# Performance work log

Hardware: AMD Instinct MI355X
Metric: run time of the kernel (lower is better)

The kernel has to match this reference:

```python
import jax, jax.numpy as jnp
import numpy as np

N = 80000       # nodes
E = 1280000     # edges (avg degree 16)
G = 2000        # graphs
NSHAPE, NCOLOR, POSMAX = 16, 16, 1024
HID, OUT, IN_DIM = 64, 2, 40
EPS = 1e-5


def setup_inputs() -> dict:
    key = jax.random.key(0)
    ks = jax.random.split(key, 20)
    f32 = jnp.float32
    return {
        "shape_id": jax.random.randint(ks[0], (N,), 0, NSHAPE),
        "color_id": jax.random.randint(ks[1], (N,), 0, NCOLOR),
        "pos_id": jax.random.randint(ks[2], (N,), 0, POSMAX),
        "edge_index": jax.random.randint(ks[3], (2, E), 0, N),
        "batch": jnp.sort(jax.random.randint(ks[4], (N,), 0, G)),
        "num_graphs": G,
        "shape_tab": jax.random.normal(ks[5], (NSHAPE, 16), f32),
        "color_tab": jax.random.normal(ks[6], (NCOLOR, 16), f32),
        "pos_tab": jax.random.normal(ks[7], (POSMAX, 8), f32),
        "W1l": jax.random.normal(ks[8], (IN_DIM, HID), f32) / np.sqrt(IN_DIM),
        "b1": jnp.zeros((HID,), f32),
        "W1r": jax.random.normal(ks[9], (IN_DIM, HID), f32) / np.sqrt(IN_DIM),
        "g1": jnp.ones((HID,), f32),
        "be1": jnp.zeros((HID,), f32),
        "W2l": jax.random.normal(ks[10], (HID, HID), f32) / np.sqrt(HID),
        "b2": jnp.zeros((HID,), f32),
        "W2r": jax.random.normal(ks[11], (HID, HID), f32) / np.sqrt(HID),
        "g2": jnp.ones((HID,), f32),
        "be2": jnp.zeros((HID,), f32),
        "Wout": jax.random.normal(ks[12], (HID, OUT), f32) / np.sqrt(HID),
        "bout": jnp.zeros((OUT,), f32),
    }


def sage_conv(x, src, dst, Wl, b, Wr, n_nodes):
    # PyG SAGEConv (mean aggr): out = lin_l(mean_{j in N(i)} x_j) + lin_r(x_i)
    agg = jax.ops.segment_sum(x[src], dst, num_segments=n_nodes)     # [N, F]
    deg = jax.ops.segment_sum(jnp.ones((src.shape[0], 1), x.dtype), dst,
                              num_segments=n_nodes)                  # [N, 1]
    agg = agg / jnp.maximum(deg, 1.0)
    return agg @ Wl + b + x @ Wr


def batch_norm(x, gamma, beta):
    # training-mode BatchNorm1d over nodes
    m = x.mean(axis=0)
    v = x.var(axis=0)
    return (x - m) * (gamma / jnp.sqrt(v + EPS)) + beta


def reference(shape_id, color_id, pos_id, edge_index, batch, num_graphs,
              shape_tab, color_tab, pos_tab,
              W1l, b1, W1r, g1, be1,
              W2l, b2, W2r, g2, be2,
              Wout, bout):
    n_nodes = shape_id.shape[0]
    src, dst = edge_index[0], edge_index[1]
    x = jnp.concatenate([shape_tab[shape_id], color_tab[color_id],
                         pos_tab[pos_id]], axis=-1)                  # [N, 40]
    x = jax.nn.relu(batch_norm(sage_conv(x, src, dst, W1l, b1, W1r, n_nodes), g1, be1))
    # dropout: eval mode -> identity
    x = jax.nn.relu(batch_norm(sage_conv(x, src, dst, W2l, b2, W2r, n_nodes), g2, be2))
    # global mean pool over batch segments
    summed = jax.ops.segment_sum(x, batch, num_segments=num_graphs)   # [G, H]
    counts = jax.ops.segment_sum(jnp.ones((n_nodes, 1), x.dtype), batch,
                                 num_segments=num_graphs)
    pooled = summed / jnp.maximum(counts, 1.0)
    return pooled @ Wout + bout                                       # [G, 2]
```

## Files before the change

### kernel.cpp

```cpp
#include <hip/hip_runtime.h>

#define NN 80000
#define NE 1280000
#define NG 2000
#define HID 64
#define FIN1 40
#define BSZ 128
#define NBUK (NN / BSZ)
#define EB 8192
#define NBB ((NE + EB - 1) / EB)
#define NBBP 160
constexpr float EPS = 1e-5f;

typedef _Float16 f16;
typedef f16 f16x8 __attribute__((ext_vector_type(8)));
typedef float f32x4 __attribute__((ext_vector_type(4)));

__global__ void setup(const int* __restrict__ sid, const int* __restrict__ cid,
                      const int* __restrict__ pid, const int* __restrict__ batch,
                      const float* __restrict__ stab, const float* __restrict__ ctab,
                      const float* __restrict__ ptab,
                      const float* __restrict__ W1l, const float* __restrict__ W1r,
                      const float* __restrict__ W2l, const float* __restrict__ W2r,
                      int* __restrict__ ids, f16* __restrict__ Bt1, f16* __restrict__ Bt2,
                      int* __restrict__ gstart,
                      f16* __restrict__ stab16, f16* __restrict__ ctab16,
                      f16* __restrict__ ptab16) {
    int bid = blockIdx.x;
    int tid = threadIdx.x;
    if (bid < 313) {
        int n = bid * 256 + tid;
        if (n < NN) ids[n] = sid[n] | (cid[n] << 4) | (pid[n] << 8);
    } else if (bid < 373) {
        int i = (bid - 313) * 256 + tid;
        if (i < 64 * 104) {
            int j = i / 104, k = i - j * 104;
            float v = 0.f;
            if (k < 40) v = W1l[k * 64 + j];
            else if (k < 80) v = W1r[(k - 40) * 64 + j];
            Bt1[i] = (f16)v;
        }
        int i2 = i - 64 * 104;
        if (i2 >= 0 && i2 < 64 * 136) {
            int j = i2 / 136, k = i2 - j * 136;
            float v = 0.f;
            if (k < 64) v = W2l[k * 64 + j];
            else if (k < 128) v = W2r[(k - 64) * 64 + j];
            Bt2[i2] = (f16)v;
        }
    } else if (bid < 686) {
        int n = (bid - 373) * 256 + tid;
        if (n >= NN) return;
        int cur = batch[n];
        int prev = (n == 0) ? -1 : batch[n - 1];
        for (int g = prev + 1; g <= cur; g++) gstart[g] = n;
        if (n == NN - 1)
            for (int g = cur + 1; g <= NG; g++) gstart[g] = NN;
    } else {
        int i = (bid - 686) * 256 + tid;
        if (i < 256) stab16[i] = (f16)stab[i];
        else if (i < 512) ctab16[i - 256] = (f16)ctab[i - 256];
        else if (i < 512 + 8192) ptab16[i - 512] = (f16)ptab[i - 512];
    }
}

__global__ void khist(const int* __restrict__ dst, int* __restrict__ bhistT,
                      int* __restrict__ bcnt) {
    __shared__ int lh[NBUK];
    for (int i = threadIdx.x; i < NBUK; i += 256) lh[i] = 0;
    __syncthreads();
    int e0 = blockIdx.x * EB, e1 = min(e0 + EB, NE);
    for (int e = e0 + threadIdx.x; e < e1; e += 256) atomicAdd(&lh[dst[e] >> 7], 1);
    __syncthreads();
    for (int i = threadIdx.x; i < NBUK; i += 256) {
        int c = lh[i];
        bhistT[i * NBBP + blockIdx.x] = c;
        if (c) atomicAdd(&bcnt[i], c);
    }
}

__global__ void kscan_a(const int* __restrict__ bcnt, int* __restrict__ bstart) {
    __shared__ int l[1024];
    int t = threadIdx.x;
    l[t] = (t < NBUK) ? bcnt[t] : 0;
    __syncthreads();
    for (int off = 1; off < 1024; off <<= 1) {
        int v = (t >= off) ? l[t - off] : 0;
        __syncthreads();
        l[t] += v;
        __syncthreads();
    }
    if (t < NBUK) bstart[t] = (t == 0) ? 0 : l[t - 1];
    if (t == NBUK) bstart[NBUK] = NE;
}

__global__ void kscan_b(const int* __restrict__ bhistT, const int* __restrict__ bstart,
                        int* __restrict__ lbaseT) {
    int b = blockIdx.x;
    int l = threadIdx.x;
    int run = bstart[b];
    for (int i0 = 0; i0 < NBB; i0 += 64) {
        int idx = i0 + l;
        int v = (idx < NBB) ? bhistT[b * NBBP + idx] : 0;
        int inc = v;
        for (int off = 1; off < 64; off <<= 1) {
            int tt = __shfl_up(inc, off);
            if (l >= off) inc += tt;
        }
        if (idx < NBB) lbaseT[b * NBBP + idx] = run + inc - v;
        run += __shfl(inc, 63);
    }
}

__global__ void kbin(const int* __restrict__ src, const int* __restrict__ dst,
                     const int* __restrict__ lbaseT, int* __restrict__ ebuf) {
    __shared__ int lcur[NBUK];
    for (int i = threadIdx.x; i < NBUK; i += 256) lcur[i] = lbaseT[i * NBBP + blockIdx.x];
    __syncthreads();
    int e0 = blockIdx.x * EB, e1 = min(e0 + EB, NE);
    for (int e = e0 + threadIdx.x; e < e1; e += 256) {
        int d = dst[e];
        int off = atomicAdd(&lcur[d >> 7], 1);
        ebuf[off] = (src[e] << 7) | (d & 127);
    }
}

__global__ void kfill(const int* __restrict__ ebuf, const int* __restrict__ bstart,
                      int* __restrict__ row_ptr, int* __restrict__ eidx) {
    __shared__ int cnt[BSZ];
    __shared__ int sb[BSZ];
    __shared__ int lcur[BSZ];
    int b = blockIdx.x, t = threadIdx.x;
    int nbase = b << 7;
    if (t < BSZ) cnt[t] = 0;
    __syncthreads();
    int s0 = bstart[b], s1 = bstart[b + 1];
    for (int i = s0 + t; i < s1; i += 256) atomicAdd(&cnt[ebuf[i] & 127], 1);
    __syncthreads();
    if (t < BSZ) sb[t] = cnt[t];
    __syncthreads();
    for (int off = 1; off < BSZ; off <<= 1) {
        int v = (t >= off && t < BSZ) ? sb[t - off] : 0;
        __syncthreads();
        if (t < BSZ) sb[t] += v;
        __syncthreads();
    }
    if (t < BSZ) {
        int excl = ((t == 0) ? 0 : sb[t - 1]) + s0;
        row_ptr[nbase + t] = excl;
        lcur[t] = excl;
    }
    if (b == 0 && t == 0) row_ptr[NN] = NE;
    __syncthreads();
    for (int i = s0 + t; i < s1; i += 256) {
        int v = ebuf[i];
        int pos = atomicAdd(&lcur[v & 127], 1);
        eidx[pos] = v >> 7;
    }
}

__global__ void gather1(const int* __restrict__ row_ptr, const int* __restrict__ eidx,
                        const int* __restrict__ ids,
                        const f16* __restrict__ stab16, const f16* __restrict__ ctab16,
                        const f16* __restrict__ ptab16, f16* __restrict__ agg) {
    int tt = blockIdx.x * 256 + threadIdx.x;
    int n = tt >> 6;
    int lane = threadIdx.x & 63;
    if (n >= NN) return;
    int grp = lane >> 3, li = lane & 7;
    int beg = row_ptr[n], end = row_ptr[n + 1];
    float ac[8];
#pragma unroll
    for (int i = 0; i < 8; i++) ac[i] = 0.f;
    for (int j0 = beg; j0 < end; j0 += 64) {
        int cnt = min(64, end - j0);
        int myid = (j0 + lane < end) ? eidx[j0 + lane] : 0;
        int steps = (cnt + 7) >> 3;
        for (int u = 0; u < steps; u++) {
            int e = u * 8 + grp;
            int s = __shfl(myid, e);
            if (e < cnt && li < 5) {
                int id = ids[s];
                const f16* rowp;
                if (li < 2)      rowp = &stab16[(id & 15) * 16 + li * 8];
                else if (li < 4) rowp = &ctab16[((id >> 4) & 15) * 16 + (li - 2) * 8];
                else             rowp = &ptab16[(id >> 8) * 8];
                f16x8 v = *(const f16x8*)rowp;
#pragma unroll
                for (int i = 0; i < 8; i++) ac[i] += (float)v[i];
            }
        }
    }
#pragma unroll
    for (int m = 8; m <= 32; m <<= 1) {
#pragma unroll
        for (int i = 0; i < 8; i++) ac[i] += __shfl_xor(ac[i], m);
    }
    if (lane < 5) {
        f16x8 o;
#pragma unroll
        for (int i = 0; i < 8; i++) o[i] = (f16)ac[i];
        *(f16x8*)&agg[(size_t)n * FIN1 + lane * 8] = o;
    }
}

__global__ void gather2(const int* __restrict__ row_ptr, const int* __restrict__ eidx,
                        const f16* __restrict__ x, const float* __restrict__ stats,
                        const float* __restrict__ g1, const float* __restrict__ be1,
                        f16* __restrict__ agg) {
    int tt = blockIdx.x * 256 + threadIdx.x;
    int n = tt >> 6;
    int lane = threadIdx.x & 63;
    if (n >= NN) return;
    int grp = lane >> 3;
    int fl = (lane & 7) * 8;
    float sc8[8], sh8[8];
    {
        const float invn = 1.0f / (float)NN;
#pragma unroll
        for (int i = 0; i < 8; i++) {
            float m = stats[fl + i] * invn;
            float var = stats[64 + fl + i] * invn - m * m;
            float sc = g1[fl + i] * __frsqrt_rn(var + EPS);
            sc8[i] = sc;
            sh8[i] = be1[fl + i] - m * sc;
        }
    }
    int beg = row_ptr[n], end = row_ptr[n + 1];
    float ac[8];
#pragma unroll
    for (int i = 0; i < 8; i++) ac[i] = 0.f;
    for (int j0 = beg; j0 < end; j0 += 64) {
        int cnt = min(64, end - j0);
        int myid = (j0 + lane < end) ? eidx[j0 + lane] : 0;
        int steps = (cnt + 7) >> 3;
        for (int u = 0; u < steps; u++) {
            int e = u * 8 + grp;
            int s = __shfl(myid, e);
            if (e < cnt) {
                f16x8 v = *(const f16x8*)&x[(size_t)s * HID + fl];
#pragma unroll
                for (int i = 0; i < 8; i++)
                    ac[i] += fmaxf(fmaf((float)v[i], sc8[i], sh8[i]), 0.f);
            }
        }
    }
#pragma unroll
    for (int m = 8; m <= 32; m <<= 1) {
#pragma unroll
        for (int i = 0; i < 8; i++) ac[i] += __shfl_xor(ac[i], m);
    }
    if (lane < 8) {
        f16x8 o;
#pragma unroll
        for (int i = 0; i < 8; i++) o[i] = (f16)ac[i];
        *(f16x8*)&agg[(size_t)n * HID + fl] = o;
    }
}

__launch_bounds__(256)
__global__ void sage_mfma1(const int* __restrict__ ids, const f16* __restrict__ agg,
                           const int* __restrict__ row_ptr,
                           const f16* __restrict__ stab16, const f16* __restrict__ ctab16,
                           const f16* __restrict__ ptab16,
                           const f16* __restrict__ Btg, const float* __restrict__ bias,
                           f16* __restrict__ h, float* __restrict__ stats) {
    const int KTOT = 96, KP = 104, UT = KP / 8;
    __shared__ f16 Asm[64 * KP];
    __shared__ f16 Bsm[64 * KP];
    __shared__ float sinv[64];
    __shared__ float sred[4][64];
    __shared__ float qred[4][64];

    int tid = threadIdx.x;
    int n0 = blockIdx.x * 64;
    if (tid < 64) {
        int n = n0 + tid;
        int deg = row_ptr[n + 1] - row_ptr[n];
        sinv[tid] = 1.0f / (float)max(deg, 1);
    }
    __syncthreads();

    for (int i = tid; i < 64 * UT; i += 256) {
        int r = i / UT, u = i - r * UT;
        f16x8 o;
        if (u < 5) {
            f16x8 va = *(const f16x8*)&agg[(size_t)(n0 + r) * FIN1 + u * 8];
            float inv = sinv[r];
#pragma unroll
            for (int k = 0; k < 8; k++) o[k] = (f16)((float)va[k] * inv);
        } else if (u < 10) {
            int id = ids[n0 + r];
            int c = u - 5;
            const f16* rowp;
            if (c < 2)      rowp = &stab16[(id & 15) * 16 + c * 8];
            else if (c < 4) rowp = &ctab16[((id >> 4) & 15) * 16 + (c - 2) * 8];
            else            rowp = &ptab16[(id >> 8) * 8];
            o = *(const f16x8*)rowp;
        } else {
#pragma unroll
            for (int k = 0; k < 8; k++) o[k] = (f16)0.f;
        }
        *(f16x8*)&Asm[r * KP + u * 8] = o;
    }
    for (int i = tid; i < 64 * KP * 2 / 16; i += 256)
        ((uint4*)Bsm)[i] = ((const uint4*)Btg)[i];
    __syncthreads();

    int w = tid >> 6, l = tid & 63;
    int jloc = l & 15, kg = l >> 4;
    int rbase = w * 16;
    f32x4 acc[4];
#pragma unroll
    for (int jt = 0; jt < 4; jt++) {
        float bj = bias[jt * 16 + jloc];
        acc[jt] = (f32x4){bj, bj, bj, bj};
    }
#pragma unroll
    for (int kk = 0; kk < KTOT / 32; kk++) {
        f16x8 af = *(const f16x8*)&Asm[(rbase + jloc) * KP + kk * 32 + kg * 8];
#pragma unroll
        for (int jt = 0; jt < 4; jt++) {
            f16x8 bf = *(const f16x8*)&Bsm[(jt * 16 + jloc) * KP + kk * 32 + kg * 8];
            acc[jt] = __builtin_amdgcn_mfma_f32_16x16x32_f16(af, bf, acc[jt], 0, 0, 0);
        }
    }
#pragma unroll
    for (int jt = 0; jt < 4; jt++) {
        float sv = 0.f, qv = 0.f;
#pragma unroll
        for (int reg = 0; reg < 4; reg++) {
            f16 hv = (f16)acc[jt][reg];
            int n = n0 + rbase + kg * 4 + reg;
            h[(size_t)n * HID + jt * 16 + jloc] = hv;
            float v = (float)hv;
            sv += v; qv += v * v;
        }
        sv += __shfl_xor(sv, 16); sv += __shfl_xor(sv, 32);
        qv += __shfl_xor(qv, 16); qv += __shfl_xor(qv, 32);
        if (kg == 0) { sred[w][jt * 16 + jloc] = sv; qred[w][jt * 16 + jloc] = qv; }
    }
    __syncthreads();
    if (tid < 128) {
        int f2 = tid & 63, which = tid >> 6;
        float r = which ? (qred[0][f2] + qred[1][f2] + qred[2][f2] + qred[3][f2])
                        : (sred[0][f2] + sred[1][f2] + sred[2][f2] + sred[3][f2]);
        atomicAdd(&stats[which * 64 + f2], r);
    }
}

__launch_bounds__(256)
__global__ void sage_mfma2(const f16* __restrict__ x, const f16* __restrict__ agg,
                           const int* __restrict__ row_ptr, const f16* __restrict__ Btg,
                           const float* __restrict__ bias, f16* __restrict__ h,
                           const float* __restrict__ stats1, const float* __restrict__ g1,
                           const float* __restrict__ be1, float* __restrict__ stats) {
    const int FIN = 64, KTOT = 128, KP = 136, UT = KP / 8;
    __shared__ f16 Asm[64 * KP];
    __shared__ f16 Bsm[64 * KP];
    __shared__ float sinv[64];
    __shared__ float ssc[64], ssh[64];
    __shared__ float sred[4][64];
    __shared__ float qred[4][64];

    int tid = threadIdx.x;
    int n0 = blockIdx.x * 64;
    if (tid < 64) {
        int n = n0 + tid;
        int deg = row_ptr[n + 1] - row_ptr[n];
        sinv[tid] = 1.0f / (float)max(deg, 1);
        const float invn = 1.0f / (float)NN;
        float m = stats1[tid] * invn;
        float var = stats1[64 + tid] * invn - m * m;
        float sc = g1[tid] * __frsqrt_rn(var + EPS);
        ssc[tid] = sc;
        ssh[tid] = be1[tid] - m * sc;
    }
    __syncthreads();

    for (int i = tid; i < 64 * UT; i += 256) {
        int r = i / UT, u = i - r * UT;
        f16x8 o;
        if (u < 8) {
            f16x8 va = *(const f16x8*)&agg[(size_t)(n0 + r) * FIN + u * 8];
            float inv = sinv[r];
#pragma unroll
            for (int k = 0; k < 8; k++) o[k] = (f16)((float)va[k] * inv);
        } else if (u < 16) {
            int fb = (u - 8) * 8;
            f16x8 vx = *(const f16x8*)&x[(size_t)(n0 + r) * FIN + fb];
#pragma unroll
            for (int k = 0; k < 8; k++)
                o[k] = (f16)fmaxf(fmaf((float)vx[k], ssc[fb + k], ssh[fb + k]), 0.f);
        } else {
#pragma unroll
            for (int k = 0; k < 8; k++) o[k] = (f16)0.f;
        }
        *(f16x8*)&Asm[r * KP + u * 8] = o;
    }
    for (int i = tid; i < 64 * KP * 2 / 16; i += 256)
        ((uint4*)Bsm)[i] = ((const uint4*)Btg)[i];
    __syncthreads();

    int w = tid >> 6, l = tid & 63;
    int jloc = l & 15, kg = l >> 4;
    int rbase = w * 16;
    f32x4 acc[4];
#pragma unroll
    for (int jt = 0; jt < 4; jt++) {
        float bj = bias[jt * 16 + jloc];
        acc[jt] = (f32x4){bj, bj, bj, bj};
    }
#pragma unroll
    for (int kk = 0; kk < KTOT / 32; kk++) {
        f16x8 af = *(const f16x8*)&Asm[(rbase + jloc) * KP + kk * 32 + kg * 8];
#pragma unroll
        for (int jt = 0; jt < 4; jt++) {
            f16x8 bf = *(const f16x8*)&Bsm[(jt * 16 + jloc) * KP + kk * 32 + kg * 8];
            acc[jt] = __builtin_amdgcn_mfma_f32_16x16x32_f16(af, bf, acc[jt], 0, 0, 0);
        }
    }
#pragma unroll
    for (int jt = 0; jt < 4; jt++) {
        float sv = 0.f, qv = 0.f;
#pragma unroll
        for (int reg = 0; reg < 4; reg++) {
            f16 hv = (f16)acc[jt][reg];
            int n = n0 + rbase + kg * 4 + reg;
            h[(size_t)n * HID + jt * 16 + jloc] = hv;
            float v = (float)hv;
            sv += v; qv += v * v;
        }
        sv += __shfl_xor(sv, 16); sv += __shfl_xor(sv, 32);
        qv += __shfl_xor(qv, 16); qv += __shfl_xor(qv, 32);
        if (kg == 0) { sred[w][jt * 16 + jloc] = sv; qred[w][jt * 16 + jloc] = qv; }
    }
    __syncthreads();
    if (tid < 128) {
        int f2 = tid & 63, which = tid >> 6;
        float r = which ? (qred[0][f2] + qred[1][f2] + qred[2][f2] + qred[3][f2])
                        : (sred[0][f2] + sred[1][f2] + sred[2][f2] + sred[3][f2]);
        atomicAdd(&stats[which * 64 + f2], r);
    }
}

__global__ void pool_out(const f16* __restrict__ h, const float* __restrict__ stats2,
                         const float* __restrict__ g2, const float* __restrict__ be2,
                         const int* __restrict__ gstart,
                         const float* __restrict__ Wout, const float* __restrict__ bout,
                         float* __restrict__ out) {
    int w = (blockIdx.x * blockDim.x + threadIdx.x) >> 6;
    int f = threadIdx.x & 63;
    if (w >= NG) return;
    const float invn = 1.0f / (float)NN;
    float m = stats2[f] * invn;
    float var = stats2[64 + f] * invn - m * m;
    float sc = g2[f] / sqrtf(var + EPS);
    float sh = be2[f] - m * sc;
    int n0 = gstart[w], n1 = gstart[w + 1];
    float acc = 0.f;
    for (int n = n0; n < n1; n++) {
        float v = fmaf((float)h[(size_t)n * HID + f], sc, sh);
        acc += fmaxf(v, 0.0f);
    }
    float inv = 1.0f / (float)max(n1 - n0, 1);
    float p = acc * inv;
    float a0 = p * Wout[f * 2 + 0];
    float a1 = p * Wout[f * 2 + 1];
#pragma unroll
    for (int mm = 1; mm < 64; mm <<= 1) {
        a0 += __shfl_xor(a0, mm);
        a1 += __shfl_xor(a1, mm);
    }
    if (f == 0) {
        out[w * 2 + 0] = a0 + bout[0];
        out[w * 2 + 1] = a1 + bout[1];
    }
}

extern "C" void kernel_launch(void* const* d_in, const int* in_sizes, int n_in,
                              void* d_out, int out_size, void* d_ws, size_t ws_size,
                              hipStream_t stream) {
    const int* sid = (const int*)d_in[0];
    const int* cid = (const int*)d_in[1];
    const int* pid = (const int*)d_in[2];
    const int* ei = (const int*)d_in[3];
    const int* batch = (const int*)d_in[4];
    const float* stab = (const float*)d_in[6];
    const float* ctab = (const float*)d_in[7];
    const float* ptab = (const float*)d_in[8];
    const float* W1l = (const float*)d_in[9];
    const float* b1 = (const float*)d_in[10];
    const float* W1r = (const float*)d_in[11];
    const float* g1 = (const float*)d_in[12];
    const float* be1 = (const float*)d_in[13];
    const float* W2l = (const float*)d_in[14];
    const float* b2 = (const float*)d_in[15];
    const float* W2r = (const float*)d_in[16];
    const float* g2 = (const float*)d_in[17];
    const float* be2 = (const float*)d_in[18];
    const float* Wout = (const float*)d_in[19];
    const float* bout = (const float*)d_in[20];

    const int* src = ei;
    const int* dst = ei + NE;

    char* p = (char*)d_ws;
    f16* agg = (f16*)p;        p += (size_t)NN * HID * 2;
    f16* h1 = (f16*)p;         p += (size_t)NN * HID * 2;
    f16* h2 = (f16*)p;         p += (size_t)NN * HID * 2;
    f16* bt1 = (f16*)p;        p += 64 * 104 * 2;
    f16* bt2 = (f16*)p;        p += 64 * 136 * 2;
    f16* stab16 = (f16*)p;     p += 256 * 2;
    f16* ctab16 = (f16*)p;     p += 256 * 2;
    f16* ptab16 = (f16*)p;     p += 8192 * 2;
    float* stats = (float*)p;  p += 256 * 4;
    int* bcnt = (int*)p;       p += NBUK * 4;
    int* ids = (int*)p;        p += (size_t)NN * 4;
    int* row_ptr = (int*)p;    p += (NN + 1) * 4;
    int* gstart = (int*)p;     p += (NG + 1) * 4;
    int* bstart = (int*)p;     p += (NBUK + 1) * 4;
    int* bhistT = (int*)p;     p += (size_t)NBUK * NBBP * 4;
    int* lbaseT = (int*)p;     p += (size_t)NBUK * NBBP * 4;
    int* ebuf = (int*)p;       p += (size_t)NE * 4;
    int* eidx = (int*)p;       p += (size_t)NE * 4;

    hipMemsetAsync(stats, 0, 256 * 4 + NBUK * 4, stream);

    const int B = 256;

    setup<<<720, B, 0, stream>>>(sid, cid, pid, batch, stab, ctab, ptab,
                                 W1l, W1r, W2l, W2r,
                                 ids, bt1, bt2, gstart, stab16, ctab16, ptab16);

    khist<<<NBB, B, 0, stream>>>(dst, bhistT, bcnt);
    kscan_a<<<1, 1024, 0, stream>>>(bcnt, bstart);
    kscan_b<<<NBUK, 64, 0, stream>>>(bhistT, bstart, lbaseT);
    kbin<<<NBB, B, 0, stream>>>(src, dst, lbaseT, ebuf);
    kfill<<<NBUK, B, 0, stream>>>(ebuf, bstart, row_ptr, eidx);

    gather1<<<(NN * 64 + B - 1) / B, B, 0, stream>>>(row_ptr, eidx, ids,
                                                     stab16, ctab16, ptab16, agg);
    sage_mfma1<<<NN / 64, B, 0, stream>>>(ids, agg, row_ptr, stab16, ctab16, ptab16,
                                          bt1, b1, h1, stats);

    gather2<<<(NN * 64 + B - 1) / B, B, 0, stream>>>(row_ptr, eidx, h1, stats, g1, be1, agg);
    sage_mfma2<<<NN / 64, B, 0, stream>>>(h1, agg, row_ptr, bt2, b2, h2,
                                          stats, g1, be1, stats + 128);

    pool_out<<<(NG * 64 + B - 1) / B, B, 0, stream>>>(h2, stats + 128, g2, be2, gstart,
                                                      Wout, bout, (float*)d_out);
}
```

Baseline: 237.9 us.

## Load MFMA operands directly from global memory and fold mean division into gathers

```diff
diff --git a/kernel.cpp b/kernel.cpp
--- a/kernel.cpp
+++ b/kernel.cpp
@@ -197,9 +197,10 @@
         for (int i = 0; i < 8; i++) ac[i] += __shfl_xor(ac[i], m);
     }
     if (lane < 5) {
+        float inv = 1.0f / (float)max(end - beg, 1);
         f16x8 o;
 #pragma unroll
-        for (int i = 0; i < 8; i++) o[i] = (f16)ac[i];
+        for (int i = 0; i < 8; i++) o[i] = (f16)(ac[i] * inv);
         *(f16x8*)&agg[(size_t)n * FIN1 + lane * 8] = o;
     }
 }
@@ -251,65 +252,50 @@
         for (int i = 0; i < 8; i++) ac[i] += __shfl_xor(ac[i], m);
     }
     if (lane < 8) {
+        float inv = 1.0f / (float)max(end - beg, 1);
         f16x8 o;
 #pragma unroll
-        for (int i = 0; i < 8; i++) o[i] = (f16)ac[i];
+        for (int i = 0; i < 8; i++) o[i] = (f16)(ac[i] * inv);
         *(f16x8*)&agg[(size_t)n * HID + fl] = o;
     }
 }
 
 __launch_bounds__(256)
-__global__ void sage_mfma1(const int* __restrict__ ids, const f16* __restrict__ agg,
-                           const int* __restrict__ row_ptr,
+__global__ void sage_mfma1(const int* __restrict__ ids, const f16* __restrict__ aggv,
                            const f16* __restrict__ stab16, const f16* __restrict__ ctab16,
                            const f16* __restrict__ ptab16,
                            const f16* __restrict__ Btg, const float* __restrict__ bias,
                            f16* __restrict__ h, float* __restrict__ stats) {
-    const int KTOT = 96, KP = 104, UT = KP / 8;
-    __shared__ f16 Asm[64 * KP];
-    __shared__ f16 Bsm[64 * KP];
-    __shared__ float sinv[64];
     __shared__ float sred[4][64];
     __shared__ float qred[4][64];
+    const int KP = 104;
 
     int tid = threadIdx.x;
     int n0 = blockIdx.x * 64;
-    if (tid < 64) {
-        int n = n0 + tid;
-        int deg = row_ptr[n + 1] - row_ptr[n];
-        sinv[tid] = 1.0f / (float)max(deg, 1);
-    }
-    __syncthreads();
-
-    for (int i = tid; i < 64 * UT; i += 256) {
-        int r = i / UT, u = i - r * UT;
-        f16x8 o;
-        if (u < 5) {
-            f16x8 va = *(const f16x8*)&agg[(size_t)(n0 + r) * FIN1 + u * 8];
-            float inv = sinv[r];
-#pragma unroll
-            for (int k = 0; k < 8; k++) o[k] = (f16)((float)va[k] * inv);
-        } else if (u < 10) {
-            int id = ids[n0 + r];
-            int c = u - 5;
-            const f16* rowp;
-            if (c < 2)      rowp = &stab16[(id & 15) * 16 + c * 8];
-            else if (c < 4) rowp = &ctab16[((id >> 4) & 15) * 16 + (c - 2) * 8];
-            else            rowp = &ptab16[(id >> 8) * 8];
-            o = *(const f16x8*)rowp;
-        } else {
-#pragma unroll
-            for (int k = 0; k < 8; k++) o[k] = (f16)0.f;
-        }
-        *(f16x8*)&Asm[r * KP + u * 8] = o;
-    }
-    for (int i = tid; i < 64 * KP * 2 / 16; i += 256)
-        ((uint4*)Bsm)[i] = ((const uint4*)Btg)[i];
-    __syncthreads();
-
     int w = tid >> 6, l = tid & 63;
     int jloc = l & 15, kg = l >> 4;
-    int rbase = w * 16;
+    int n = n0 + w * 16 + jloc;
+
+    f16x8 af[3];
+#pragma unroll
+    for (int kk = 0; kk < 3; kk++) {
+        int c = kk * 4 + kg;
+        if (c < 5) {
+            af[kk] = *(const f16x8*)&aggv[(size_t)n * FIN1 + c * 8];
+        } else if (c < 10) {
+            int id = ids[n];
+            int cc = c - 5;
+            const f16* rowp;
+            if (cc < 2)      rowp = &stab16[(id & 15) * 16 + cc * 8];
+            else if (cc < 4) rowp = &ctab16[((id >> 4) & 15) * 16 + (cc - 2) * 8];
+            else             rowp = &ptab16[(id >> 8) * 8];
+            af[kk] = *(const f16x8*)rowp;
+        } else {
+#pragma unroll
+            for (int i = 0; i < 8; i++) af[kk][i] = (f16)0.f;
+        }
+    }
+
     f32x4 acc[4];
 #pragma unroll
     for (int jt = 0; jt < 4; jt++) {
@@ -317,12 +303,11 @@
         acc[jt] = (f32x4){bj, bj, bj, bj};
     }
 #pragma unroll
-    for (int kk = 0; kk < KTOT / 32; kk++) {
-        f16x8 af = *(const f16x8*)&Asm[(rbase + jloc) * KP + kk * 32 + kg * 8];
+    for (int kk = 0; kk < 3; kk++) {
 #pragma unroll
         for (int jt = 0; jt < 4; jt++) {
-            f16x8 bf = *(const f16x8*)&Bsm[(jt * 16 + jloc) * KP + kk * 32 + kg * 8];
-            acc[jt] = __builtin_amdgcn_mfma_f32_16x16x32_f16(af, bf, acc[jt], 0, 0, 0);
+            f16x8 bf = *(const f16x8*)&Btg[(jt * 16 + jloc) * KP + kk * 32 + kg * 8];
+            acc[jt] = __builtin_amdgcn_mfma_f32_16x16x32_f16(af[kk], bf, acc[jt], 0, 0, 0);
         }
     }
 #pragma unroll
@@ -331,8 +316,8 @@
 #pragma unroll
         for (int reg = 0; reg < 4; reg++) {
             f16 hv = (f16)acc[jt][reg];
-            int n = n0 + rbase + kg * 4 + reg;
-            h[(size_t)n * HID + jt * 16 + jloc] = hv;
+            int nn2 = n0 + w * 16 + kg * 4 + reg;
+            h[(size_t)nn2 * HID + jt * 16 + jloc] = hv;
             float v = (float)hv;
             sv += v; qv += v * v;
         }
@@ -350,25 +335,19 @@
 }
 
 __launch_bounds__(256)
-__global__ void sage_mfma2(const f16* __restrict__ x, const f16* __restrict__ agg,
-                           const int* __restrict__ row_ptr, const f16* __restrict__ Btg,
-                           const float* __restrict__ bias, f16* __restrict__ h,
+__global__ void sage_mfma2(const f16* __restrict__ x, const f16* __restrict__ aggv,
+                           const f16* __restrict__ Btg, const float* __restrict__ bias,
+                           f16* __restrict__ h,
                            const float* __restrict__ stats1, const float* __restrict__ g1,
                            const float* __restrict__ be1, float* __restrict__ stats) {
-    const int FIN = 64, KTOT = 128, KP = 136, UT = KP / 8;
-    __shared__ f16 Asm[64 * KP];
-    __shared__ f16 Bsm[64 * KP];
-    __shared__ float sinv[64];
     __shared__ float ssc[64], ssh[64];
     __shared__ float sred[4][64];
     __shared__ float qred[4][64];
+    const int KP = 136;
 
     int tid = threadIdx.x;
     int n0 = blockIdx.x * 64;
     if (tid < 64) {
-        int n = n0 + tid;
-        int deg = row_ptr[n + 1] - row_ptr[n];
-        sinv[tid] = 1.0f / (float)max(deg, 1);
         const float invn = 1.0f / (float)NN;
         float m = stats1[tid] * invn;
         float var = stats1[64 + tid] * invn - m * m;
@@ -378,33 +357,25 @@
     }
     __syncthreads();
 
-    for (int i = tid; i < 64 * UT; i += 256) {
-        int r = i / UT, u = i - r * UT;
-        f16x8 o;
-        if (u < 8) {
-            f16x8 va = *(const f16x8*)&agg[(size_t)(n0 + r) * FIN + u * 8];
-            float inv = sinv[r];
-#pragma unroll
-            for (int k = 0; k < 8; k++) o[k] = (f16)((float)va[k] * inv);
-        } else if (u < 16) {
-            int fb = (u - 8) * 8;
-            f16x8 vx = *(const f16x8*)&x[(size_t)(n0 + r) * FIN + fb];
-#pragma unroll
-            for (int k = 0; k < 8; k++)
-                o[k] = (f16)fmaxf(fmaf((float)vx[k], ssc[fb + k], ssh[fb + k]), 0.f);
-        } else {
-#pragma unroll
-            for (int k = 0; k < 8; k++) o[k] = (f16)0.f;
-        }
-        *(f16x8*)&Asm[r * KP + u * 8] = o;
-    }
-    for (int i = tid; i < 64 * KP * 2 / 16; i += 256)
-        ((uint4*)Bsm)[i] = ((const uint4*)Btg)[i];
-    __syncthreads();
-
     int w = tid >> 6, l = tid & 63;
     int jloc = l & 15, kg = l >> 4;
-    int rbase = w * 16;
+    int n = n0 + w * 16 + jloc;
+
+    f16x8 af[4];
+#pragma unroll
+    for (int kk = 0; kk < 4; kk++) {
+        int c = kk * 4 + kg;
+        if (c < 8) {
+            af[kk] = *(const f16x8*)&aggv[(size_t)n * HID + c * 8];
+        } else {
+            int fb = (c - 8) * 8;
+            f16x8 vx = *(const f16x8*)&x[(size_t)n * HID + fb];
+#pragma unroll
+            for (int i = 0; i < 8; i++)
+                af[kk][i] = (f16)fmaxf(fmaf((float)vx[i], ssc[fb + i], ssh[fb + i]), 0.f);
+        }
+    }
+
     f32x4 acc[4];
 #pragma unroll
     for (int jt = 0; jt < 4; jt++) {
@@ -412,12 +383,11 @@
         acc[jt] = (f32x4){bj, bj, bj, bj};
     }
 #pragma unroll
-    for (int kk = 0; kk < KTOT / 32; kk++) {
-        f16x8 af = *(const f16x8*)&Asm[(rbase + jloc) * KP + kk * 32 + kg * 8];
+    for (int kk = 0; kk < 4; kk++) {
 #pragma unroll
         for (int jt = 0; jt < 4; jt++) {
-            f16x8 bf = *(const f16x8*)&Bsm[(jt * 16 + jloc) * KP + kk * 32 + kg * 8];
-            acc[jt] = __builtin_amdgcn_mfma_f32_16x16x32_f16(af, bf, acc[jt], 0, 0, 0);
+            f16x8 bf = *(const f16x8*)&Btg[(jt * 16 + jloc) * KP + kk * 32 + kg * 8];
+            acc[jt] = __builtin_amdgcn_mfma_f32_16x16x32_f16(af[kk], bf, acc[jt], 0, 0, 0);
         }
     }
 #pragma unroll
@@ -426,8 +396,8 @@
 #pragma unroll
         for (int reg = 0; reg < 4; reg++) {
             f16 hv = (f16)acc[jt][reg];
-            int n = n0 + rbase + kg * 4 + reg;
-            h[(size_t)n * HID + jt * 16 + jloc] = hv;
+            int nn2 = n0 + w * 16 + kg * 4 + reg;
+            h[(size_t)nn2 * HID + jt * 16 + jloc] = hv;
             float v = (float)hv;
             sv += v; qv += v * v;
         }
@@ -541,11 +511,11 @@
 
     gather1<<<(NN * 64 + B - 1) / B, B, 0, stream>>>(row_ptr, eidx, ids,
                                                      stab16, ctab16, ptab16, agg);
-    sage_mfma1<<<NN / 64, B, 0, stream>>>(ids, agg, row_ptr, stab16, ctab16, ptab16,
+    sage_mfma1<<<NN / 64, B, 0, stream>>>(ids, agg, stab16, ctab16, ptab16,
                                           bt1, b1, h1, stats);
 
     gather2<<<(NN * 64 + B - 1) / B, B, 0, stream>>>(row_ptr, eidx, h1, stats, g1, be1, agg);
-    sage_mfma2<<<NN / 64, B, 0, stream>>>(h1, agg, row_ptr, bt2, b2, h2,
+    sage_mfma2<<<NN / 64, B, 0, stream>>>(h1, agg, bt2, b2, h2,
                                           stats, g1, be1, stats + 128);
 
     pool_out<<<(NG * 64 + B - 1) / B, B, 0, stream>>>(h2, stats + 128, g2, be2, gstart,
```

Result: no change. 234.1 us (-1.6%).
